# Kernel optimization log

Hardware: AMD Instinct MI355X
Metric: run time of the kernel (lower is better)

Reference implementation:

```python
import jax, jax.numpy as jnp
import numpy as np

BITS = 4
GROUP_SIZE = 128
INF, OUTF, TOKENS = 4096, 11008, 256


def setup_inputs() -> dict:
    key = jax.random.key(0)
    k1, k2, k3, k4, k5 = jax.random.split(key, 5)
    n_groups = INF // GROUP_SIZE  # 32
    x = jax.random.normal(k1, (TOKENS, INF), dtype=jnp.float32)
    qweight = jax.random.randint(k2, (INF // 32 * BITS, OUTF), 0, 2**31 - 1, dtype=jnp.int32)
    qzeros = jax.random.randint(k3, (n_groups, OUTF // 32 * BITS), 0, 2**31 - 1, dtype=jnp.int32)
    scales = jax.random.uniform(k4, (n_groups, OUTF), dtype=jnp.float32, minval=1e-3, maxval=2e-2)
    bias = jax.random.normal(k5, (OUTF,), dtype=jnp.float32)
    return {"x": x, "qweight": qweight, "qzeros": qzeros, "scales": scales, "bias": bias}


def _dequantize(qweight, qzeros, scales):
    """Unpack int4 nibbles and build the fp32 weight [infeatures, outfeatures]."""
    shifts = jnp.arange(0, 32, BITS, dtype=jnp.int32)  # [8]
    mask = (1 << BITS) - 1
    out_f = qweight.shape[1]
    # qweight row packs 8 consecutive in-features -> [K, O] int in [0, 15]
    w = ((qweight[:, None, :] >> shifts[None, :, None]) & mask).reshape(-1, out_f)
    # qzeros col packs 8 consecutive out-features; stored as (zero - 1)
    n_groups = qzeros.shape[0]
    z = (((qzeros[:, :, None] >> shifts[None, None, :]) & mask) + 1).reshape(n_groups, out_f)
    g_idx = jnp.arange(w.shape[0], dtype=jnp.int32) // GROUP_SIZE  # [K]
    return (w - z[g_idx]).astype(jnp.float32) * scales[g_idx]


def reference(x, qweight, qzeros, scales, bias):
    W = _dequantize(qweight, qzeros, scales)  # [infeatures, outfeatures]
    return x @ W + bias  # [tokens, outfeatures]
```

## Files before the change

### kernel.cpp

```cpp
#include <hip/hip_runtime.h>
#include <stdint.h>

#define TOKENS  256
#define INF     4096
#define OUTF    11008
#define NGROUPS 32
#define KSPLIT  2
#define PHK     128
#define NPH     ((INF / KSPLIT) / PHK)
#define NTH     256

typedef __attribute__((ext_vector_type(2))) _Float16 f16x2;
typedef __attribute__((ext_vector_type(8))) _Float16 f16x8;
typedef __attribute__((ext_vector_type(2))) __fp16   pkh2;
typedef __attribute__((ext_vector_type(4))) float    f32x4;

union U32H2 { uint32_t u; f16x2 h; };
union H8    { f16x2 h2[4]; f16x8 h8; };
union PK    { pkh2 p; f16x2 h; };

__device__ __forceinline__ void gl2lds16(const void* g, void* l) {
    __builtin_amdgcn_global_load_lds(
        (const __attribute__((address_space(1))) uint32_t*)g,
        (__attribute__((address_space(3))) uint32_t*)l, 16, 0, 0);
}

__global__ __launch_bounds__(NTH)
void cvt_x(const float* __restrict__ x, _Float16* __restrict__ x16) {
    const int t   = blockIdx.x * NTH + threadIdx.x;
    const int row = t >> 9;
    const int c   = t & 511;
    const float* p = x + (size_t)row * INF + c * 8;
    f32x4 v0 = *(const f32x4*)p;
    f32x4 v1 = *(const f32x4*)(p + 4);
    H8 o; PK k0, k1, k2, k3;
    k0.p = __builtin_amdgcn_cvt_pkrtz(v0[0], v1[0]);
    k1.p = __builtin_amdgcn_cvt_pkrtz(v0[1], v1[1]);
    k2.p = __builtin_amdgcn_cvt_pkrtz(v0[2], v1[2]);
    k3.p = __builtin_amdgcn_cvt_pkrtz(v0[3], v1[3]);
    o.h2[0] = k0.h; o.h2[1] = k1.h; o.h2[2] = k2.h; o.h2[3] = k3.h;
    *(f16x8*)(x16 + (size_t)row * INF + c * 8) = o.h8;
}

__global__ __launch_bounds__(NTH)
void init_out(const float* __restrict__ bias, float* __restrict__ out) {
    const int t = blockIdx.x * NTH + threadIdx.x;
    const int c = t % (OUTF / 4);
    const int r = t / (OUTF / 4);
    const f32x4 b = ((const f32x4*)bias)[c];
    ((f32x4*)out)[(size_t)r * (OUTF / 4) + c] = b;
}

__global__ __launch_bounds__(NTH, 3)
void qlin_main(const _Float16* __restrict__ x16,
               const uint32_t* __restrict__ qweight,
               const uint32_t* __restrict__ qzeros,
               const float* __restrict__ scales,
               float* __restrict__ out)
{
    __shared__ alignas(16) _Float16 As[2][64 * PHK];

    const int tid = threadIdx.x;

    const int d  = blockIdx.x;
    const int cx = d & 7, kk = d >> 3;
    int strip, memb;
    if (kk < 80) { strip = cx * 10 + (kk >> 3); memb = kk & 7; }
    else         { const int t2 = ((kk - 80) << 3) | cx; strip = 80 + (t2 >> 3); memb = t2 & 7; }
    const int bx = strip;
    const int by = memb >> 1;
    const int ks = memb & 1;

    const int lane = tid & 63;
    const int quad = lane >> 4;
    const int l16  = lane & 15;
    const int wv   = tid >> 6;

    const int rowoff = tid >> 4;
    const int chk    = tid & 15;
    const int row0   = by * 64;
    const uint32_t aoff = (uint32_t)((row0 + rowoff) * (INF * 2)
                                     + ks * (INF / KSPLIT) * 2
                                     + ((chk ^ rowoff) & 15) * 16);
    const char* x16b = (const char*)x16;
    _Float16* ldsW = &As[0][0];
    const int ldsSlotBase = wv * 512;

    const int col0 = bx * 128 + wv * 32 + l16;
    const int col1 = col0 + 16;
    const int bOff0 = quad * OUTF + col0;
    const int bOff1 = quad * OUTF + col1;
    const int zsh   = (col0 & 7) * 4;
    const int qrow0 = ks * (INF / KSPLIT / 8);
    const int g0    = ks * (NGROUPS / KSPLIT);

    f32x4 acc[4][2];
#pragma unroll
    for (int mi = 0; mi < 4; ++mi)
#pragma unroll
        for (int nf = 0; nf < 2; ++nf)
            acc[mi][nf] = f32x4{0.f, 0.f, 0.f, 0.f};

    uint32_t Breg[2][8];
    float    sS[2][2];
    uint32_t qZ[2][2];

#pragma unroll
    for (int r = 0; r < 4; ++r)
        gl2lds16(x16b + aoff + r * 131072, ldsW + r * 2048 + ldsSlotBase);
    {
        const uint32_t* qp = qweight + (size_t)qrow0 * OUTF;
#pragma unroll
        for (int s = 0; s < 4; ++s) {
            Breg[0][2 * s + 0] = qp[(size_t)(s * 4) * OUTF + bOff0];
            Breg[0][2 * s + 1] = qp[(size_t)(s * 4) * OUTF + bOff1];
        }
        sS[0][0] = scales[g0 * OUTF + col0];
        sS[0][1] = scales[g0 * OUTF + col1];
        qZ[0][0] = qzeros[g0 * (OUTF / 8) + (col0 >> 3)];
        qZ[0][1] = qzeros[g0 * (OUTF / 8) + (col1 >> 3)];
    }
    __syncthreads();

#define PHASE_BODY(PAR, P, DO_PREFETCH)                                          \
    {                                                                            \
        const int p_ = (P);                                                      \
        if (DO_PREFETCH) {                                                       \
            const int pn = p_ + 1;                                               \
            const uint32_t pb = (uint32_t)(pn * (PHK * 2));                      \
            _Float16* ldsN = ldsW + (1 - (PAR)) * 8192;                          \
            _Pragma("unroll")                                                    \
            for (int r = 0; r < 4; ++r)                                          \
                gl2lds16(x16b + aoff + r * 131072 + pb,                          \
                         ldsN + r * 2048 + ldsSlotBase);                         \
            const uint32_t* qpb = qweight + (size_t)(qrow0 + pn * 16) * OUTF;    \
            _Pragma("unroll")                                                    \
            for (int s = 0; s < 4; ++s) {                                        \
                Breg[1 - (PAR)][2 * s + 0] = qpb[(size_t)(s * 4) * OUTF + bOff0];\
                Breg[1 - (PAR)][2 * s + 1] = qpb[(size_t)(s * 4) * OUTF + bOff1];\
            }                                                                    \
            const int gn = g0 + pn;                                              \
            sS[1 - (PAR)][0] = scales[gn * OUTF + col0];                         \
            sS[1 - (PAR)][1] = scales[gn * OUTF + col1];                         \
            qZ[1 - (PAR)][0] = qzeros[gn * (OUTF / 8) + (col0 >> 3)];            \
            qZ[1 - (PAR)][1] = qzeros[gn * (OUTF / 8) + (col1 >> 3)];            \
        }                                                                        \
        f16x2 hs2[2], hz2[2];                                                    \
        _Pragma("unroll")                                                        \
        for (int nf = 0; nf < 2; ++nf) {                                         \
            const float s = sS[PAR][nf];                                         \
            const int   z = (int)((qZ[PAR][nf] >> zsh) & 15u) + 1025;            \
            const _Float16 hs = (_Float16)s;                                     \
            const _Float16 hz = (_Float16)(-(float)z);                           \
            hs2[nf] = f16x2{hs, hs};                                             \
            hz2[nf] = f16x2{hz, hz};                                             \
        }                                                                        \
        const _Float16* buf = ldsW + (PAR) * 8192;                               \
        _Pragma("unroll")                                                        \
        for (int s = 0; s < 4; ++s) {                                            \
            f16x8 af[4];                                                         \
            _Pragma("unroll")                                                    \
            for (int mi = 0; mi < 4; ++mi) {                                     \
                const int m  = mi * 16 + l16;                                    \
                const int sc = ((s * 4 + quad) ^ l16) & 15;                      \
                af[mi] = *(const f16x8*)(buf + m * PHK + sc * 8);                \
            }                                                                    \
            _Pragma("unroll")                                                    \
            for (int nf = 0; nf < 2; ++nf) {                                     \
                const uint32_t q = Breg[PAR][2 * s + nf];                        \
                H8 b;                                                            \
                _Pragma("unroll")                                                \
                for (int j = 0; j < 4; ++j) {                                    \
                    U32H2 u;                                                     \
                    u.u = ((q >> (4 * j)) & 0x000F000Fu) | 0x64006400u;          \
                    b.h2[j] = (u.h + hz2[nf]) * hs2[nf];                         \
                }                                                                \
                _Pragma("unroll")                                                \
                for (int mi = 0; mi < 4; ++mi)                                   \
                    acc[mi][nf] = __builtin_amdgcn_mfma_f32_16x16x32_f16(        \
                        af[mi], b.h8, acc[mi][nf], 0, 0, 0);                     \
            }                                                                    \
        }                                                                        \
        __syncthreads();                                                         \
    }

#pragma unroll 1
    for (int pp = 0; pp < NPH / 2; ++pp) {
        PHASE_BODY(0, 2 * pp, true)
        PHASE_BODY(1, 2 * pp + 1, (pp < NPH / 2 - 1))
    }
#undef PHASE_BODY

#pragma unroll
    for (int nf = 0; nf < 2; ++nf) {
        const int col = (nf == 0) ? col0 : col1;
#pragma unroll
        for (int mi = 0; mi < 4; ++mi) {
            const int r0 = by * 64 + mi * 16 + quad * 4;
#pragma unroll
            for (int rg = 0; rg < 4; ++rg)
                unsafeAtomicAdd(&out[(size_t)(r0 + rg) * OUTF + col],
                                acc[mi][nf][rg]);
        }
    }
}

__global__ __launch_bounds__(NTH, 2)
void qlin_fb(const float* __restrict__ x,
             const uint32_t* __restrict__ qweight,
             const uint32_t* __restrict__ qzeros,
             const float* __restrict__ scales,
             const float* __restrict__ bias,
             float* __restrict__ out)
{
    __shared__ alignas(16) _Float16 Asb[64][40];
    __shared__ alignas(16) _Float16 Bsb[128][40];
    const int tid = threadIdx.x;
    const int bx = blockIdx.x, by = blockIdx.y;
    const int am = tid >> 2, ar = tid & 3;
    const float* xrow = x + (size_t)(by * 64 + am) * INF + ar * 8;
    const int bc = tid & 127, br = tid >> 7;
    const int bn = bx * 128 + bc;
    const int bswz = (bc >> 3) & 3;
    const int lane = tid & 63, quad = lane >> 4, l16 = lane & 15;
    const int wv = tid >> 6, wm = wv >> 1, wn = wv & 1;
    f32x4 acc[2][4];
#pragma unroll
    for (int i = 0; i < 2; ++i)
#pragma unroll
        for (int j = 0; j < 4; ++j) acc[i][j] = f32x4{0.f, 0.f, 0.f, 0.f};
    f32x4 pa0 = *(const f32x4*)(xrow + 0);
    f32x4 pa1 = *(const f32x4*)(xrow + 4);
    uint32_t pq0 = qweight[(size_t)br * OUTF + bn];
    uint32_t pq1 = qweight[(size_t)(br + 2) * OUTF + bn];
    for (int g = 0; g < NGROUPS; ++g) {
        const float s = scales[g * OUTF + bn];
        const uint32_t qzv = qzeros[g * (OUTF / 8) + (bn >> 3)];
        const int z = (int)((qzv >> (4 * (bn & 7))) & 15u) + 1;
        const _Float16 hs = (_Float16)s;
        const _Float16 hz = (_Float16)(-(float)(1024 + z));
        const f16x2 hs2 = {hs, hs}, hz2 = {hz, hz};
#pragma unroll
        for (int t4 = 0; t4 < 4; ++t4) {
            const int it = (g << 2) + t4;
            { H8 ah; PK p0, p1, p2, p3;
              p0.p = __builtin_amdgcn_cvt_pkrtz(pa0[0], pa1[0]);
              p1.p = __builtin_amdgcn_cvt_pkrtz(pa0[1], pa1[1]);
              p2.p = __builtin_amdgcn_cvt_pkrtz(pa0[2], pa1[2]);
              p3.p = __builtin_amdgcn_cvt_pkrtz(pa0[3], pa1[3]);
              ah.h2[0] = p0.h; ah.h2[1] = p1.h; ah.h2[2] = p2.h; ah.h2[3] = p3.h;
              *(f16x8*)&Asb[am][ar * 8] = ah.h8; }
            { const uint32_t qq[2] = {pq0, pq1};
#pragma unroll
              for (int rr = 0; rr < 2; ++rr) {
                  const int r = br + rr * 2; H8 bh;
#pragma unroll
                  for (int jp = 0; jp < 4; ++jp) {
                      U32H2 u; u.u = ((qq[rr] >> (4 * jp)) & 0x000F000Fu) | 0x64006400u;
                      bh.h2[jp] = (u.h + hz2) * hs2;
                  }
                  *(f16x8*)&Bsb[bc][(r ^ bswz) * 8] = bh.h8;
              } }
            __syncthreads();
            const int itn = (it < 127) ? it + 1 : 127;
            pa0 = *(const f32x4*)(xrow + itn * 32);
            pa1 = *(const f32x4*)(xrow + itn * 32 + 4);
            pq0 = qweight[(size_t)(itn * 4 + br) * OUTF + bn];
            pq1 = qweight[(size_t)(itn * 4 + br + 2) * OUTF + bn];
            f16x8 af[2], bf[4];
#pragma unroll
            for (int mi = 0; mi < 2; ++mi)
                af[mi] = *(const f16x8*)&Asb[wm * 32 + mi * 16 + l16][quad * 8];
#pragma unroll
            for (int ni = 0; ni < 4; ++ni) {
                const int c = wn * 64 + ni * 16 + l16;
                bf[ni] = *(const f16x8*)&Bsb[c][(quad ^ ((c >> 3) & 3)) * 8];
            }
#pragma unroll
            for (int mi = 0; mi < 2; ++mi)
#pragma unroll
                for (int ni = 0; ni < 4; ++ni)
                    acc[mi][ni] = __builtin_amdgcn_mfma_f32_16x16x32_f16(
                        af[mi], bf[ni], acc[mi][ni], 0, 0, 0);
            __syncthreads();
        }
    }
#pragma unroll
    for (int ni = 0; ni < 4; ++ni) {
        const int col = bx * 128 + wn * 64 + ni * 16 + l16;
        const float bv = bias[col];
#pragma unroll
        for (int mi = 0; mi < 2; ++mi) {
            const int row0 = by * 64 + wm * 32 + mi * 16 + quad * 4;
#pragma unroll
            for (int rg = 0; rg < 4; ++rg)
                out[(size_t)(row0 + rg) * OUTF + col] = acc[mi][ni][rg] + bv;
        }
    }
}

extern "C" void kernel_launch(void* const* d_in, const int* in_sizes, int n_in,
                              void* d_out, int out_size, void* d_ws, size_t ws_size,
                              hipStream_t stream) {
    const float*    xx = (const float*)d_in[0];
    const uint32_t* qw = (const uint32_t*)d_in[1];
    const uint32_t* qz = (const uint32_t*)d_in[2];
    const float*    sc = (const float*)d_in[3];
    const float*    bs = (const float*)d_in[4];
    float* out = (float*)d_out;

    const size_t x16_bytes = (size_t)TOKENS * INF * sizeof(_Float16);
    if (ws_size >= x16_bytes) {
        _Float16* x16 = (_Float16*)d_ws;
        init_out<<<(TOKENS * OUTF / 4) / NTH, NTH, 0, stream>>>(bs, out);
        cvt_x<<<(TOKENS * INF / 8) / NTH, NTH, 0, stream>>>(xx, x16);
        qlin_main<<<(OUTF / 128) * (TOKENS / 64) * KSPLIT, NTH, 0, stream>>>(
            x16, qw, qz, sc, out);
    } else {
        dim3 grid(OUTF / 128, TOKENS / 64);
        qlin_fb<<<grid, NTH, 0, stream>>>(xx, qw, qz, sc, bs, out);
    }
}
```

Baseline: 123.7 us.

## Merge prep kernels and restructure main-loop sync with partial vmcnt waits

```diff
diff --git a/kernel.cpp b/kernel.cpp
--- a/kernel.cpp
+++ b/kernel.cpp
@@ -26,29 +26,30 @@
 }
 
 __global__ __launch_bounds__(NTH)
-void cvt_x(const float* __restrict__ x, _Float16* __restrict__ x16) {
-    const int t   = blockIdx.x * NTH + threadIdx.x;
-    const int row = t >> 9;
-    const int c   = t & 511;
-    const float* p = x + (size_t)row * INF + c * 8;
-    f32x4 v0 = *(const f32x4*)p;
-    f32x4 v1 = *(const f32x4*)(p + 4);
-    H8 o; PK k0, k1, k2, k3;
-    k0.p = __builtin_amdgcn_cvt_pkrtz(v0[0], v1[0]);
-    k1.p = __builtin_amdgcn_cvt_pkrtz(v0[1], v1[1]);
-    k2.p = __builtin_amdgcn_cvt_pkrtz(v0[2], v1[2]);
-    k3.p = __builtin_amdgcn_cvt_pkrtz(v0[3], v1[3]);
-    o.h2[0] = k0.h; o.h2[1] = k1.h; o.h2[2] = k2.h; o.h2[3] = k3.h;
-    *(f16x8*)(x16 + (size_t)row * INF + c * 8) = o.h8;
-}
-
-__global__ __launch_bounds__(NTH)
-void init_out(const float* __restrict__ bias, float* __restrict__ out) {
-    const int t = blockIdx.x * NTH + threadIdx.x;
-    const int c = t % (OUTF / 4);
-    const int r = t / (OUTF / 4);
-    const f32x4 b = ((const f32x4*)bias)[c];
-    ((f32x4*)out)[(size_t)r * (OUTF / 4) + c] = b;
+void prep(const float* __restrict__ x, _Float16* __restrict__ x16,
+          const float* __restrict__ bias, float* __restrict__ out) {
+    const int b = blockIdx.x;
+    if (b < 512) {
+        const int t   = b * NTH + threadIdx.x;
+        const int row = t >> 9;
+        const int c   = t & 511;
+        const float* p = x + (size_t)row * INF + c * 8;
+        f32x4 v0 = *(const f32x4*)p;
+        f32x4 v1 = *(const f32x4*)(p + 4);
+        H8 o; PK k0, k1, k2, k3;
+        k0.p = __builtin_amdgcn_cvt_pkrtz(v0[0], v1[0]);
+        k1.p = __builtin_amdgcn_cvt_pkrtz(v0[1], v1[1]);
+        k2.p = __builtin_amdgcn_cvt_pkrtz(v0[2], v1[2]);
+        k3.p = __builtin_amdgcn_cvt_pkrtz(v0[3], v1[3]);
+        o.h2[0] = k0.h; o.h2[1] = k1.h; o.h2[2] = k2.h; o.h2[3] = k3.h;
+        *(f16x8*)(x16 + (size_t)row * INF + c * 8) = o.h8;
+    } else {
+        const int t = (b - 512) * NTH + threadIdx.x;
+        const int c = t % (OUTF / 4);
+        const int r = t / (OUTF / 4);
+        const f32x4 bv = ((const f32x4*)bias)[c];
+        ((f32x4*)out)[(size_t)r * (OUTF / 4) + c] = bv;
+    }
 }
 
 __global__ __launch_bounds__(NTH, 3)
@@ -108,42 +109,46 @@
 #pragma unroll
     for (int r = 0; r < 4; ++r)
         gl2lds16(x16b + aoff + r * 131072, ldsW + r * 2048 + ldsSlotBase);
+    __builtin_amdgcn_sched_barrier(0);
     {
+        sS[0][0] = scales[g0 * OUTF + col0];
+        sS[0][1] = scales[g0 * OUTF + col1];
+        qZ[0][0] = qzeros[g0 * (OUTF / 8) + (col0 >> 3)];
+        qZ[0][1] = qzeros[g0 * (OUTF / 8) + (col1 >> 3)];
         const uint32_t* qp = qweight + (size_t)qrow0 * OUTF;
 #pragma unroll
         for (int s = 0; s < 4; ++s) {
             Breg[0][2 * s + 0] = qp[(size_t)(s * 4) * OUTF + bOff0];
             Breg[0][2 * s + 1] = qp[(size_t)(s * 4) * OUTF + bOff1];
         }
-        sS[0][0] = scales[g0 * OUTF + col0];
-        sS[0][1] = scales[g0 * OUTF + col1];
-        qZ[0][0] = qzeros[g0 * (OUTF / 8) + (col0 >> 3)];
-        qZ[0][1] = qzeros[g0 * (OUTF / 8) + (col1 >> 3)];
-    }
-    __syncthreads();
+    }
 
 #define PHASE_BODY(PAR, P, DO_PREFETCH)                                          \
     {                                                                            \
-        const int p_ = (P);                                                      \
+        __builtin_amdgcn_sched_barrier(0);                                       \
+        asm volatile("s_waitcnt vmcnt(8)" ::: "memory");                         \
+        __builtin_amdgcn_s_barrier();                                            \
+        __builtin_amdgcn_sched_barrier(0);                                       \
         if (DO_PREFETCH) {                                                       \
-            const int pn = p_ + 1;                                               \
+            const int pn = (P) + 1;                                              \
             const uint32_t pb = (uint32_t)(pn * (PHK * 2));                      \
             _Float16* ldsN = ldsW + (1 - (PAR)) * 8192;                          \
             _Pragma("unroll")                                                    \
             for (int r = 0; r < 4; ++r)                                          \
                 gl2lds16(x16b + aoff + r * 131072 + pb,                          \
                          ldsN + r * 2048 + ldsSlotBase);                         \
+            __builtin_amdgcn_sched_barrier(0);           \
+            const int gn = g0 + pn;                                              \
+            sS[1 - (PAR)][0] = scales[gn * OUTF + col0];                         \
+            sS[1 - (PAR)][1] = scales[gn * OUTF + col1];                         \
+            qZ[1 - (PAR)][0] = qzeros[gn * (OUTF / 8) + (col0 >> 3)];            \
+            qZ[1 - (PAR)][1] = qzeros[gn * (OUTF / 8) + (col1 >> 3)];            \
             const uint32_t* qpb = qweight + (size_t)(qrow0 + pn * 16) * OUTF;    \
             _Pragma("unroll")                                                    \
             for (int s = 0; s < 4; ++s) {                                        \
                 Breg[1 - (PAR)][2 * s + 0] = qpb[(size_t)(s * 4) * OUTF + bOff0];\
                 Breg[1 - (PAR)][2 * s + 1] = qpb[(size_t)(s * 4) * OUTF + bOff1];\
             }                                                                    \
-            const int gn = g0 + pn;                                              \
-            sS[1 - (PAR)][0] = scales[gn * OUTF + col0];                         \
-            sS[1 - (PAR)][1] = scales[gn * OUTF + col1];                         \
-            qZ[1 - (PAR)][0] = qzeros[gn * (OUTF / 8) + (col0 >> 3)];            \
-            qZ[1 - (PAR)][1] = qzeros[gn * (OUTF / 8) + (col1 >> 3)];            \
         }                                                                        \
         f16x2 hs2[2], hz2[2];                                                    \
         _Pragma("unroll")                                                        \
@@ -175,13 +180,14 @@
                     u.u = ((q >> (4 * j)) & 0x000F000Fu) | 0x64006400u;          \
                     b.h2[j] = (u.h + hz2[nf]) * hs2[nf];                         \
                 }                                                                \
+                __builtin_amdgcn_s_setprio(1);                                   \
                 _Pragma("unroll")                                                \
                 for (int mi = 0; mi < 4; ++mi)                                   \
                     acc[mi][nf] = __builtin_amdgcn_mfma_f32_16x16x32_f16(        \
                         af[mi], b.h8, acc[mi][nf], 0, 0, 0);                     \
+                __builtin_amdgcn_s_setprio(0);                                   \
             }                                                                    \
         }                                                                        \
-        __syncthreads();                                                         \
     }
 
 #pragma unroll 1
@@ -312,8 +318,7 @@
     const size_t x16_bytes = (size_t)TOKENS * INF * sizeof(_Float16);
     if (ws_size >= x16_bytes) {
         _Float16* x16 = (_Float16*)d_ws;
-        init_out<<<(TOKENS * OUTF / 4) / NTH, NTH, 0, stream>>>(bs, out);
-        cvt_x<<<(TOKENS * INF / 8) / NTH, NTH, 0, stream>>>(xx, x16);
+        prep<<<512 + (TOKENS * OUTF / 4) / NTH, NTH, 0, stream>>>(xx, x16, bs, out);
         qlin_main<<<(OUTF / 128) * (TOKENS / 64) * KSPLIT, NTH, 0, stream>>>(
             x16, qw, qz, sc, out);
     } else {
```

Result: no change. 122.2 us (-1.3%).
